# Kernel tuning notes

Hardware: AMD Instinct MI355X
Metric: run time of the kernel (lower is better)

The kernel has to match this reference:

```python
import jax, jax.numpy as jnp
import numpy as np

B, H, W = 16, 256, 256
C = 64          # width
M1, M2 = 12, 12 # retained Fourier modes
FC_HID = 128


def setup_inputs() -> dict:
    key = jax.random.key(0)
    ks = jax.random.split(key, 10)
    scale = 1.0 / (C * C)
    inp = {
        "x": jax.random.normal(ks[0], (B, H, W, 1), dtype=jnp.float32),
        "fc0_w": jax.random.normal(ks[1], (1, C), dtype=jnp.float32) * (1.0 / np.sqrt(1)),
        "fc0_b": jnp.zeros((C,), dtype=jnp.float32),
        # 4 layers x {weights1, weights2} x [Cin, Cout, M1, M2] x {re, im}
        "sc_w": jax.random.uniform(ks[2], (4, 2, C, C, M1, M2, 2), dtype=jnp.float32) * scale,
        # 1x1 conv weights [layer, Cout, Cin] and biases [layer, Cout]
        "pw_w": jax.random.normal(ks[3], (4, C, C), dtype=jnp.float32) * (1.0 / np.sqrt(C)),
        "pw_b": jnp.zeros((4, C), dtype=jnp.float32),
        "fc1_w": jax.random.normal(ks[4], (C, FC_HID), dtype=jnp.float32) * (1.0 / np.sqrt(C)),
        "fc1_b": jnp.zeros((FC_HID,), dtype=jnp.float32),
        "fc2_w": jax.random.normal(ks[5], (FC_HID, 1), dtype=jnp.float32) * (1.0 / np.sqrt(FC_HID)),
        "fc2_b": jnp.zeros((1,), dtype=jnp.float32),
    }
    return inp


def _spectral_conv(x, w1, w2):
    # x: [B, C, H, W] real; w1, w2: [Cin, Cout, M1, M2] complex
    xf = jnp.fft.rfft2(x, axes=(-2, -1))                # [B, C, H, W//2+1]
    top = jnp.einsum('bixy,ioxy->boxy', xf[:, :, :M1, :M2], w1)
    bot = jnp.einsum('bixy,ioxy->boxy', xf[:, :, -M1:, :M2], w2)
    out_ft = jnp.zeros((x.shape[0], w1.shape[1], x.shape[2], x.shape[3] // 2 + 1),
                       dtype=jnp.complex64)
    out_ft = out_ft.at[:, :, :M1, :M2].set(top)
    out_ft = out_ft.at[:, :, -M1:, :M2].set(bot)
    return jnp.fft.irfft2(out_ft, s=(x.shape[2], x.shape[3]), axes=(-2, -1))


def _gelu(x):
    return jax.nn.gelu(x, approximate=False)  # torch F.gelu default = exact erf


def reference(x, fc0_w, fc0_b, sc_w, pw_w, pw_b, fc1_w, fc1_b, fc2_w, fc2_b):
    # lift: [B,H,W,1] -> [B,H,W,C] -> [B,C,H,W]
    h = jnp.einsum('bhwi,ic->bhwc', x, fc0_w) + fc0_b
    h = jnp.transpose(h, (0, 3, 1, 2))
    scw = sc_w[..., 0] + 1j * sc_w[..., 1]  # [4, 2, C, C, M1, M2] complex
    for l in range(4):
        x1 = _spectral_conv(h, scw[l, 0], scw[l, 1])
        x2 = jnp.einsum('bihw,oi->bohw', h, pw_w[l]) + pw_b[l][None, :, None, None]
        h = x1 + x2
        if l < 3:
            h = _gelu(h)
    h = jnp.transpose(h, (0, 2, 3, 1))  # [B,H,W,C]
    h = _gelu(jnp.einsum('bhwc,cd->bhwd', h, fc1_w) + fc1_b)
    out = jnp.einsum('bhwd,do->bhwo', h, fc2_w) + fc2_b
    return out
```

## Files before the change

kernel.cpp:

```cpp
#include <hip/hip_runtime.h>
#include <hip/hip_bf16.h>
#include <math.h>

#define Hn 256
#define Wn 256
#define Cn 64
#define Mk 12
#define NM 24
#define FCH 128
#define HW 65536

using half8 = __attribute__((ext_vector_type(8))) _Float16;
using f32x4 = __attribute__((ext_vector_type(4))) float;

__device__ __forceinline__ float gelu_exact(float x) {
    return 0.5f * x * (1.0f + erff(x * 0.7071067811865476f));
}
__device__ __forceinline__ unsigned short f2h(float f) {
    _Float16 h = (_Float16)f;
    return __builtin_bit_cast(unsigned short, h);
}

__global__ __launch_bounds__(256) void k_init_tables(float* tc, float* ts,
                                                     float* twc, float* tws,
                                                     float* tcs,
                                                     unsigned short* bfr,
                                                     unsigned short* tfr) {
    int i = threadIdx.x;
    const float step = 0.024543692606170259f;
    float c = cosf(i * step), s = sinf(i * step);
    tc[i] = c; ts[i] = s;
    tcs[2 * i] = c; tcs[2 * i + 1] = s;
    for (int k = 0; k < Mk; ++k) {
        int idx = (i * k) & 255;
        twc[i * Mk + k] = cosf(idx * step);
        tws[i * Mk + k] = sinf(idx * step);
    }
    for (int e = i; e < 8192; e += 256) {
        int j  = e & 7;
        int l  = (e >> 3) & 63;
        int sn = e >> 9;
        int col = (sn & 1) * 16 + (l & 15);
        int ky = col >> 1, p = col & 1;
        int k  = (sn >> 1) * 32 + ((l >> 4) & 3) * 8 + j;
        int idx = (ky * k) & 255;
        float v = p ? -sinf(idx * step) : cosf(idx * step);
        bfr[e] = f2h(v);
    }
    for (int e = i; e < 12288; e += 256) {
        int j  = e & 7;
        int l  = (e >> 3) & 63;
        int sm = e >> 9;
        int mt = sm % 3, s2 = sm / 3;
        int r  = mt * 16 + (l & 15);
        int hh = s2 * 32 + ((l >> 4) & 3) * 8 + j;
        int m  = (r < 24) ? r : (r - 24);
        int kx = (m < Mk) ? m : (232 + m);
        int idx = (kx * hh) & 255;
        float v = (r < 24) ? cosf(idx * step) : sinf(idx * step);
        tfr[e] = f2h(v);
    }
}

__global__ __launch_bounds__(256) void k_prep_frag(const float* __restrict__ pww,
                                                   const float* __restrict__ fc1w,
                                                   unsigned short* __restrict__ efr,
                                                   unsigned short* __restrict__ pwfr,
                                                   unsigned short* __restrict__ fc1fr) {
    int e = blockIdx.x * 256 + threadIdx.x;
    const float step = 0.024543692606170259f;
    int j = e & 7, l = (e >> 3) & 63;
    int row = l & 15;
    int k = ((l >> 4) & 3) * 8 + j;
    if (e < 8192) {
        int mt = (e >> 9) & 15;
        int pix = mt * 16 + row;
        float v = 0.f;
        if (k < 12) v = cosf(((k * pix) & 255) * step);
        else if (k < 24) v = -sinf((((k - 12) * pix) & 255) * step);
        efr[e] = f2h(v);
    } else if (e < 24576) {
        int e2 = e - 8192;
        int nt = (e2 >> 9) & 3;
        int ks = (e2 >> 11) & 1;
        int l4 = e2 >> 12;
        int o = nt * 16 + row;
        int i = ks * 32 + k;
        pwfr[e2] = f2h(pww[(size_t)(l4 * 64 + o) * 64 + i]);
    } else {
        int e2 = e - 24576;
        int nt = (e2 >> 9) & 7;
        int ks = (e2 >> 12) & 1;
        int d = nt * 16 + row;
        int i = ks * 32 + k;
        fc1fr[e2] = f2h(fc1w[i * 128 + d]);
    }
}

__global__ __launch_bounds__(256) void k_prep_wfrag(const float* __restrict__ scw,
                                                    unsigned short* __restrict__ wfr) {
    __shared__ float Ws[8192];
    int mat = blockIdx.x;
    int lj = mat / 144, kxw = (mat / 12) % 12, ky = mat % 12;
    int t = threadIdx.x;
    const float* base = scw + (((size_t)lj * 4096) * 144 + kxw * 12 + ky) * 2;
#pragma unroll
    for (int r = 0; r < 16; ++r) {
        int idx = r * 256 + t;
        float2 v = *(const float2*)(base + (size_t)idx * 288);
        Ws[idx * 2] = v.x; Ws[idx * 2 + 1] = v.y;
    }
    __syncthreads();
    unsigned short* dst = wfr + (size_t)mat * 16384;
#pragma unroll
    for (int u = 0; u < 8; ++u) {
        int lin = u * 256 + t;
        int lane = lin & 63, nt = (lin >> 6) & 7, s = lin >> 9;
        int col = nt * 16 + (lane & 15);
        int o = col >> 1, pp = col & 1;
        int tg = (lane >> 4) & 3;
        unsigned pk[4];
#pragma unroll
        for (int jp = 0; jp < 4; ++jp) {
            unsigned short hv[2];
#pragma unroll
            for (int hz = 0; hz < 2; ++hz) {
                int k = s * 32 + tg * 8 + jp * 2 + hz;
                int i = k >> 1, p = k & 1;
                float wr_ = Ws[(i * 64 + o) * 2];
                float wi_ = Ws[(i * 64 + o) * 2 + 1];
                float v = (p == 0) ? (pp == 0 ? wr_ : wi_)
                                   : (pp == 0 ? -wi_ : wr_);
                hv[hz] = f2h(v);
            }
            pk[jp] = hv[0] | ((unsigned)hv[1] << 16);
        }
        uint4 w4 = {pk[0], pk[1], pk[2], pk[3]};
        *(uint4*)(dst + lin * 8) = w4;
    }
}

__global__ __launch_bounds__(64) void k_dftw_x(const float* __restrict__ x,
                                               float* __restrict__ Xxw,
                                               const float* __restrict__ twc,
                                               const float* __restrict__ tws) {
    int r = blockIdx.x * 64 + threadIdx.x;
    const float* hp = x + (size_t)r * Wn;
    float xr[Mk], xi[Mk];
#pragma unroll
    for (int k = 0; k < Mk; ++k) { xr[k] = 0.f; xi[k] = 0.f; }
    for (int w4 = 0; w4 < 64; ++w4) {
        float4 v = ((const float4*)hp)[w4];
        float vv[4] = {v.x, v.y, v.z, v.w};
#pragma unroll
        for (int j = 0; j < 4; ++j) {
            int wbase = (w4 * 4 + j) * Mk;
#pragma unroll
            for (int k = 0; k < Mk; ++k) {
                xr[k] += vv[j] * twc[wbase + k];
                xi[k] -= vv[j] * tws[wbase + k];
            }
        }
    }
    float* op = Xxw + (size_t)r * (2 * Mk);
#pragma unroll
    for (int k = 0; k < Mk; ++k) { op[2 * k] = xr[k]; op[2 * k + 1] = xi[k]; }
}

__global__ __launch_bounds__(256) void k_xdfth(const float* __restrict__ Xxw,
                                               float* __restrict__ Xfx,
                                               const float* __restrict__ tc,
                                               const float* __restrict__ ts) {
    int t = blockIdx.x * 256 + threadIdx.x;
    if (t >= 16 * 288) return;
    int ky = t % Mk;
    int m  = (t / Mk) % NM;
    int b  = t / 288;
    int kx = (m < Mk) ? m : (232 + m);
    const float* base = Xxw + (size_t)b * Hn * 2 * Mk + 2 * ky;
    float ar = 0.f, ai = 0.f;
    for (int hh = 0; hh < Hn; ++hh) {
        float vr = base[hh * 2 * Mk];
        float vi = base[hh * 2 * Mk + 1];
        int idx = (kx * hh) & 255;
        float c = tc[idx], s = ts[idx];
        ar += vr * c + vi * s;
        ai += vi * c - vr * s;
    }
    Xfx[2 * t] = ar;
    Xfx[2 * t + 1] = ai;
}

__global__ __launch_bounds__(256) void k_mixZ2(const float* __restrict__ xin,
                                               const unsigned short* __restrict__ wfr,
                                               const float* __restrict__ w0,
                                               const float* __restrict__ b0v,
                                               float* __restrict__ Z,
                                               int l, int first, int b0, int bc) {
    __shared__ __align__(16) char smem[4096];
    int t = threadIdx.x;
    int lane = t & 63, q = t >> 6, tg = (lane >> 4) & 3;
    int blk2 = blockIdx.x;
    int hlf = blk2 & 1;
    int blk = blk2 >> 1;
    int jj = blk / 144, kxw = (blk / 12) % 12, ky = blk % 12;
    int mm = jj * 12 + kxw;
    int mk = mm * 12 + ky;
    int mat = (l * 2 + jj) * 144 + kxw * 12 + ky;
    {
        int b = t >> 4, c16 = t & 15;
        uint4 pk = {0u, 0u, 0u, 0u};
        if (b < bc) {
            if (first) {
                float xr = xin[((b0 + b) * 288 + mk) * 2] * 0.0625f;
                float xi = xin[((b0 + b) * 288 + mk) * 2 + 1] * 0.0625f;
                float4 wv = *(const float4*)(w0 + c16 * 4);
                float4 bv = {0.f, 0.f, 0.f, 0.f};
                if (mk == 0) {
                    float4 bb = *(const float4*)(b0v + c16 * 4);
                    bv.x = 4096.f * bb.x; bv.y = 4096.f * bb.y;
                    bv.z = 4096.f * bb.z; bv.w = 4096.f * bb.w;
                }
                pk.x = f2h(wv.x * xr + bv.x) | ((unsigned)f2h(wv.x * xi) << 16);
                pk.y = f2h(wv.y * xr + bv.y) | ((unsigned)f2h(wv.y * xi) << 16);
                pk.z = f2h(wv.z * xr + bv.z) | ((unsigned)f2h(wv.z * xi) << 16);
                pk.w = f2h(wv.w * xr + bv.w) | ((unsigned)f2h(wv.w * xi) << 16);
            } else {
                const float* src = xin + ((size_t)b * 288 + mk) * 128 + c16 * 8;
                float4 v0 = *(const float4*)(src);
                float4 v1 = *(const float4*)(src + 4);
                pk.x = f2h(v0.x * 0.0625f) | ((unsigned)f2h(v0.y * 0.0625f) << 16);
                pk.y = f2h(v0.z * 0.0625f) | ((unsigned)f2h(v0.w * 0.0625f) << 16);
                pk.z = f2h(v1.x * 0.0625f) | ((unsigned)f2h(v1.y * 0.0625f) << 16);
                pk.w = f2h(v1.z * 0.0625f) | ((unsigned)f2h(v1.w * 0.0625f) << 16);
            }
        }
        *(uint4*)(smem + ((b * 256 + c16 * 16) ^ ((b & 7) << 4))) = pk;
    }
    __syncthreads();
    int nt = hlf * 4 + q;
    const uint4* bt = (const uint4*)wfr + (size_t)mat * 2048;
    f32x4 ac = {0.f, 0.f, 0.f, 0.f};
    int brow = lane & 15;
#pragma unroll
    for (int s = 0; s < 4; ++s) {
        half8 af = *(const half8*)(smem + ((brow * 256 + s * 64 + tg * 16) ^ ((brow & 7) << 4)));
        half8 bf = __builtin_bit_cast(half8, bt[(s * 8 + nt) * 64 + lane]);
        ac = __builtin_amdgcn_mfma_f32_16x16x32_f16(af, bf, ac, 0, 0, 0);
    }
    const float sc = 16.0f * 2.0f / 65536.0f;
    int col = nt * 16 + (lane & 15);
    int o = col >> 1, pp = col & 1;
#pragma unroll
    for (int r = 0; r < 4; ++r) {
        int bb = (lane >> 4) * 4 + r;
        if (bb < bc)
            Z[(((size_t)bb * 12 + ky) * 64 + o) * 48 + mm * 2 + pp] = ac[r] * sc;
    }
}

__global__ __launch_bounds__(256) void k_dfth(const float* __restrict__ Xw,
                                              float* __restrict__ Xf2,
                                              const unsigned short* __restrict__ tfr) {
    __shared__ __align__(16) char smem[65536];
    int b = blockIdx.x / 12, ky = blockIdx.x % 12;
    int t = threadIdx.x;
    int lane = t & 63, q = t >> 6;
    const float* P = Xw + ((size_t)b * 12 + ky) * 32768;
    int c = lane;
#pragma unroll 4
    for (int k = 0; k < 32; ++k) {
        int hh0 = k * 8 + q * 2;
        float2 a  = *(const float2*)(P + hh0 * 128 + 2 * c);
        float2 bv = *(const float2*)(P + (hh0 + 1) * 128 + 2 * c);
        unsigned int u0 = f2h(a.x * 0.0625f) | ((unsigned int)f2h(bv.x * 0.0625f) << 16);
        unsigned int u1 = f2h(a.y * 0.0625f) | ((unsigned int)f2h(bv.y * 0.0625f) << 16);
        int ch0 = 2 * c, ch1 = 2 * c + 1;
        *(unsigned int*)(smem + ch0 * 512 + ((2 * hh0) ^ ((ch0 & 7) << 4))) = u0;
        *(unsigned int*)(smem + ch1 * 512 + ((2 * hh0) ^ ((ch1 & 7) << 4))) = u1;
    }
    __syncthreads();
    int ct0 = q * 2;
    int tg = (lane >> 4) & 3;
    f32x4 a00 = {0,0,0,0}, a01 = {0,0,0,0}, a10 = {0,0,0,0};
    f32x4 a11 = {0,0,0,0}, a20 = {0,0,0,0}, a21 = {0,0,0,0};
    const uint4* tf4 = (const uint4*)tfr;
#pragma unroll
    for (int s = 0; s < 8; ++s) {
        half8 af0 = __builtin_bit_cast(half8, tf4[(s * 3 + 0) * 64 + lane]);
        half8 af1 = __builtin_bit_cast(half8, tf4[(s * 3 + 1) * 64 + lane]);
        half8 af2 = __builtin_bit_cast(half8, tf4[(s * 3 + 2) * 64 + lane]);
        int chan0 = ct0 * 16 + (lane & 15);
        int chan1 = chan0 + 16;
        int off = s * 64 + tg * 16;
        half8 b0 = *(const half8*)(smem + chan0 * 512 + (off ^ ((chan0 & 7) << 4)));
        half8 b1 = *(const half8*)(smem + chan1 * 512 + (off ^ ((chan1 & 7) << 4)));
        a00 = __builtin_amdgcn_mfma_f32_16x16x32_f16(af0, b0, a00, 0, 0, 0);
        a01 = __builtin_amdgcn_mfma_f32_16x16x32_f16(af0, b1, a01, 0, 0, 0);
        a10 = __builtin_amdgcn_mfma_f32_16x16x32_f16(af1, b0, a10, 0, 0, 0);
        a11 = __builtin_amdgcn_mfma_f32_16x16x32_f16(af1, b1, a11, 0, 0, 0);
        a20 = __builtin_amdgcn_mfma_f32_16x16x32_f16(af2, b0, a20, 0, 0, 0);
        a21 = __builtin_amdgcn_mfma_f32_16x16x32_f16(af2, b1, a21, 0, 0, 0);
    }
    __syncthreads();
    float* Cs = (float*)smem;
    {
        int rl = (lane >> 4) * 4;
        int chan0 = ct0 * 16 + (lane & 15);
#pragma unroll
        for (int r = 0; r < 4; ++r) {
            Cs[(0  + rl + r) * 128 + chan0]      = a00[r];
            Cs[(0  + rl + r) * 128 + chan0 + 16] = a01[r];
            Cs[(16 + rl + r) * 128 + chan0]      = a10[r];
            Cs[(16 + rl + r) * 128 + chan0 + 16] = a11[r];
            Cs[(32 + rl + r) * 128 + chan0]      = a20[r];
            Cs[(32 + rl + r) * 128 + chan0 + 16] = a21[r];
        }
    }
    __syncthreads();
#pragma unroll
    for (int k = 0; k < 6; ++k) {
        int p = t + 256 * k;
        int m = p >> 6, i = p & 63;
        float r1 = Cs[m * 128 + 2 * i];
        float i1 = Cs[m * 128 + 2 * i + 1];
        float r2 = Cs[(24 + m) * 128 + 2 * i];
        float i2 = Cs[(24 + m) * 128 + 2 * i + 1];
        ((float2*)Xf2)[((size_t)b * 288 + m * 12 + ky) * 64 + i] =
            make_float2((r1 + i2) * 16.0f, (i1 - r2) * 16.0f);
    }
}

__global__ __launch_bounds__(256, 4) void k_fusedA(const float* __restrict__ x0,
        const unsigned short* hin,
        const float* __restrict__ Zb, const float* __restrict__ pwb,
        const float* __restrict__ w0, const float* __restrict__ b0v,
        unsigned short* hout, float* __restrict__ XwOut,
        const float* __restrict__ tcs,
        const unsigned short* __restrict__ bfr,
        const unsigned short* __restrict__ efr,
        const unsigned short* __restrict__ pwfr,
        int l, int first) {
    __shared__ __align__(16) char smem[37120];
    float* Ysh = (float*)smem;
    char*  Yfr = smem + 32768;
    float* csm = (float*)(smem + 36864);
    int b  = blockIdx.x >> 8;
    int hh = blockIdx.x & 255;
    int w  = threadIdx.x;
    int lane = w & 63, q = w >> 6;
    int tg = (lane >> 4) & 3;
    const float2* tc2 = (const float2*)tcs;
    if (w < NM) {
        int kx = (w < Mk) ? w : (232 + w);
        float2 cs = tc2[(kx * hh) & 255];
        csm[2 * w] = cs.x; csm[2 * w + 1] = cs.y;
    }
    __syncthreads();
    const float* Zbb = Zb + (size_t)b * 36864;
    const float4* cs4 = (const float4*)csm;
#pragma unroll
    for (int r3 = 0; r3 < 3; ++r3) {
        int p = w + 256 * r3;
        int o = p / Mk, ky = p % Mk;
        const float4* zv = (const float4*)(Zbb + ((size_t)ky * 64 + o) * 48);
        float yr = 0.f, yi = 0.f;
#pragma unroll
        for (int mm = 0; mm < 12; ++mm) {
            float4 z  = zv[mm];
            float4 cc = cs4[mm];
            yr += z.x * cc.x - z.y * cc.y + z.z * cc.z - z.w * cc.w;
            yi += z.x * cc.y + z.y * cc.x + z.z * cc.w + z.w * cc.z;
        }
        Ysh[p * 2] = yr; Ysh[p * 2 + 1] = yi;
    }
    __syncthreads();
    {
        int o = q * 16 + (lane & 15);
        unsigned pv[4];
#pragma unroll
        for (int jp = 0; jp < 4; ++jp) {
            unsigned short h2[2];
#pragma unroll
            for (int hzz = 0; hzz < 2; ++hzz) {
                int u = tg * 8 + jp * 2 + hzz;
                float v;
                if (u == 0) v = 0.5f * Ysh[o * 24];
                else if (u < 12) v = Ysh[o * 24 + 2 * u];
                else if (u < 24) v = Ysh[o * 24 + 2 * (u - 12) + 1];
                else v = 0.f;
                h2[hzz] = f2h(v);
            }
            pv[jp] = h2[0] | ((unsigned)h2[1] << 16);
        }
        uint4 pk = {pv[0], pv[1], pv[2], pv[3]};
        *(uint4*)(Yfr + (q * 64 + lane) * 16) = pk;
    }
    __syncthreads();
    {
        int swz = (w & 7) << 4;
        if (first) {
            float xv = x0[(size_t)b * HW + hh * 256 + w];
#pragma unroll
            for (int ic = 0; ic < 4; ++ic) {
                unsigned pv[8];
#pragma unroll
                for (int j2 = 0; j2 < 16; j2 += 2) {
                    float a0 = w0[ic * 16 + j2] * xv + b0v[ic * 16 + j2];
                    float a1 = w0[ic * 16 + j2 + 1] * xv + b0v[ic * 16 + j2 + 1];
                    pv[j2 >> 1] = f2h(a0) | ((unsigned)f2h(a1) << 16);
                }
                uint4 lo = {pv[0], pv[1], pv[2], pv[3]};
                uint4 hi = {pv[4], pv[5], pv[6], pv[7]};
                *(uint4*)(smem + ((w * 128 + ic * 32) ^ swz)) = lo;
                *(uint4*)(smem + ((w * 128 + ic * 32 + 16) ^ swz)) = hi;
            }
        } else {
            const unsigned short* hb = hin + (size_t)b * Cn * HW + hh * 256 + w;
#pragma unroll
            for (int ic = 0; ic < 4; ++ic) {
                unsigned pv[8];
#pragma unroll
                for (int j2 = 0; j2 < 16; j2 += 2) {
                    unsigned a0 = hb[(size_t)(ic * 16 + j2) * HW];
                    unsigned a1 = hb[(size_t)(ic * 16 + j2 + 1) * HW];
                    pv[j2 >> 1] = a0 | (a1 << 16);
                }
                uint4 lo = {pv[0], pv[1], pv[2], pv[3]};
                uint4 hi = {pv[4], pv[5], pv[6], pv[7]};
                *(uint4*)(smem + ((w * 128 + ic * 32) ^ swz)) = lo;
                *(uint4*)(smem + ((w * 128 + ic * 32 + 16) ^ swz)) = hi;
            }
        }
    }
    __syncthreads();
    uint2 gp[4][4];
    {
        const uint4* efr4 = (const uint4*)efr;
        const uint4* pw4  = (const uint4*)pwfr;
        float biasn[4];
        half8 ybf[4]; uint4 cwa[4], cwb[4];
#pragma unroll
        for (int nt = 0; nt < 4; ++nt) {
            biasn[nt] = pwb[l * 64 + nt * 16 + (lane & 15)];
            ybf[nt] = *(const half8*)(Yfr + (nt * 64 + lane) * 16);
            cwa[nt] = pw4[((l * 2 + 0) * 4 + nt) * 64 + lane];
            cwb[nt] = pw4[((l * 2 + 1) * 4 + nt) * 64 + lane];
        }
#pragma unroll
        for (int mt = 0; mt < 4; ++mt) {
            int mtA = q * 4 + mt;
            half8 ea = __builtin_bit_cast(half8, efr4[mtA * 64 + lane]);
            int row = mtA * 16 + (lane & 15);
            int rsw = (row & 7) << 4;
            half8 a0 = *(const half8*)(smem + ((row * 128 + tg * 16) ^ rsw));
            half8 a1 = *(const half8*)(smem + ((row * 128 + 64 + tg * 16) ^ rsw));
#pragma unroll
            for (int nt = 0; nt < 4; ++nt) {
                f32x4 acc = {0.f, 0.f, 0.f, 0.f};
                acc = __builtin_amdgcn_mfma_f32_16x16x32_f16(ea, ybf[nt], acc, 0, 0, 0);
                acc = __builtin_amdgcn_mfma_f32_16x16x32_f16(a0, __builtin_bit_cast(half8, cwa[nt]), acc, 0, 0, 0);
                acc = __builtin_amdgcn_mfma_f32_16x16x32_f16(a1, __builtin_bit_cast(half8, cwb[nt]), acc, 0, 0, 0);
                float g0 = gelu_exact(acc[0] + biasn[nt]);
                float g1 = gelu_exact(acc[1] + biasn[nt]);
                float g2 = gelu_exact(acc[2] + biasn[nt]);
                float g3 = gelu_exact(acc[3] + biasn[nt]);
                gp[mt][nt].x = f2h(g0) | ((unsigned)f2h(g1) << 16);
                gp[mt][nt].y = f2h(g2) | ((unsigned)f2h(g3) << 16);
            }
        }
    }
    unsigned short* hnb = hout + (size_t)b * Cn * HW + hh * 256;
#pragma unroll
    for (int mt = 0; mt < 4; ++mt) {
        int pbase = (q * 4 + mt) * 16 + (lane >> 4) * 4;
#pragma unroll
        for (int nt = 0; nt < 4; ++nt) {
            int o = nt * 16 + (lane & 15);
            *(uint2*)(hnb + (size_t)o * HW + pbase) = gp[mt][nt];
        }
    }
    __syncthreads();
#pragma unroll
    for (int mt = 0; mt < 4; ++mt) {
        int pbase = (q * 4 + mt) * 16 + (lane >> 4) * 4;
#pragma unroll
        for (int nt = 0; nt < 4; ++nt) {
            int o = nt * 16 + (lane & 15);
            int sidx = (((pbase >> 3) ^ (o & 7)) << 3) | (pbase & 7);
            *(uint2*)(smem + o * 512 + sidx * 2) = gp[mt][nt];
        }
    }
    __syncthreads();
    {
        int arow = q * 16 + (lane & 15);
        const uint4* bt = (const uint4*)bfr;
        f32x4 ac0 = {0.f, 0.f, 0.f, 0.f};
        f32x4 ac1 = {0.f, 0.f, 0.f, 0.f};
#pragma unroll
        for (int s = 0; s < 8; ++s) {
            int abyte = (arow * 512 + s * 64 + tg * 16) ^ ((arow & 7) << 4);
            half8 af = __builtin_bit_cast(half8, *(const uint4*)(smem + abyte));
            half8 b0 = __builtin_bit_cast(half8, bt[(s * 2 + 0) * 64 + lane]);
            half8 b1 = __builtin_bit_cast(half8, bt[(s * 2 + 1) * 64 + lane]);
            ac0 = __builtin_amdgcn_mfma_f32_16x16x32_f16(af, b0, ac0, 0, 0, 0);
            ac1 = __builtin_amdgcn_mfma_f32_16x16x32_f16(af, b1, ac1, 0, 0, 0);
        }
        float* Xwb = XwOut + (size_t)b * 393216;
        int rbase = q * 16 + (lane >> 4) * 4;
#pragma unroll
        for (int n = 0; n < 2; ++n) {
            f32x4 ac = n ? ac1 : ac0;
            int col = n * 16 + (lane & 15);
            int ky = col >> 1, p = col & 1;
            if (ky < Mk) {
                float* dst = Xwb + (size_t)ky * 32768 + hh * 128 + rbase * 2 + p;
                dst[0] = ac[0]; dst[2] = ac[1]; dst[4] = ac[2]; dst[6] = ac[3];
            }
        }
    }
}

__global__ __launch_bounds__(256, 4) void k_fusedB(const unsigned short* __restrict__ hin,
        const float* __restrict__ Zb, const float* __restrict__ pwb,
        const float* __restrict__ fc1b, const float* __restrict__ fc2w,
        const float* __restrict__ fc2b, float* __restrict__ outp,
        const float* __restrict__ tcs,
        const unsigned short* __restrict__ efr,
        const unsigned short* __restrict__ pwfr,
        const unsigned short* __restrict__ fc1fr) {
    __shared__ __align__(16) char smem[37120];
    float* Ysh = (float*)smem;
    char*  Yfr = smem + 32768;
    float* csm = (float*)(smem + 36864);
    int b  = blockIdx.x >> 8;
    int hh = blockIdx.x & 255;
    int w  = threadIdx.x;
    int lane = w & 63, q = w >> 6;
    int tg = (lane >> 4) & 3;
    const float2* tc2 = (const float2*)tcs;
    if (w < NM) {
        int kx = (w < Mk) ? w : (232 + w);
        float2 cs = tc2[(kx * hh) & 255];
        csm[2 * w] = cs.x; csm[2 * w + 1] = cs.y;
    }
    __syncthreads();
    const float* Zbb = Zb + (size_t)b * 36864;
    const float4* cs4 = (const float4*)csm;
#pragma unroll
    for (int r3 = 0; r3 < 3; ++r3) {
        int p = w + 256 * r3;
        int o = p / Mk, ky = p % Mk;
        const float4* zv = (const float4*)(Zbb + ((size_t)ky * 64 + o) * 48);
        float yr = 0.f, yi = 0.f;
#pragma unroll
        for (int mm = 0; mm < 12; ++mm) {
            float4 z  = zv[mm];
            float4 cc = cs4[mm];
            yr += z.x * cc.x - z.y * cc.y + z.z * cc.z - z.w * cc.w;
            yi += z.x * cc.y + z.y * cc.x + z.z * cc.w + z.w * cc.z;
        }
        Ysh[p * 2] = yr; Ysh[p * 2 + 1] = yi;
    }
    __syncthreads();
    {
        int o = q * 16 + (lane & 15);
        unsigned pv[4];
#pragma unroll
        for (int jp = 0; jp < 4; ++jp) {
            unsigned short h2[2];
#pragma unroll
            for (int hzz = 0; hzz < 2; ++hzz) {
                int u = tg * 8 + jp * 2 + hzz;
                float v;
                if (u == 0) v = 0.5f * Ysh[o * 24];
                else if (u < 12) v = Ysh[o * 24 + 2 * u];
                else if (u < 24) v = Ysh[o * 24 + 2 * (u - 12) + 1];
                else v = 0.f;
                h2[hzz] = f2h(v);
            }
            pv[jp] = h2[0] | ((unsigned)h2[1] << 16);
        }
        uint4 pk = {pv[0], pv[1], pv[2], pv[3]};
        *(uint4*)(Yfr + (q * 64 + lane) * 16) = pk;
    }
    __syncthreads();
    {
        int swz = (w & 7) << 4;
        const unsigned short* hb = hin + (size_t)b * Cn * HW + hh * 256 + w;
#pragma unroll
        for (int ic = 0; ic < 4; ++ic) {
            unsigned pv[8];
#pragma unroll
            for (int j2 = 0; j2 < 16; j2 += 2) {
                unsigned a0 = hb[(size_t)(ic * 16 + j2) * HW];
                unsigned a1 = hb[(size_t)(ic * 16 + j2 + 1) * HW];
                pv[j2 >> 1] = a0 | (a1 << 16);
            }
            uint4 lo = {pv[0], pv[1], pv[2], pv[3]};
            uint4 hi = {pv[4], pv[5], pv[6], pv[7]};
            *(uint4*)(smem + ((w * 128 + ic * 32) ^ swz)) = lo;
            *(uint4*)(smem + ((w * 128 + ic * 32 + 16) ^ swz)) = hi;
        }
    }
    __syncthreads();
    uint2 R2[16];
    {
        const uint4* efr4 = (const uint4*)efr;
        const uint4* pw4 = (const uint4*)pwfr;
        half8 ay  = *(const half8*)(Yfr + (q * 64 + lane) * 16);
        half8 aw0 = __builtin_bit_cast(half8, pw4[((3 * 2 + 0) * 4 + q) * 64 + lane]);
        half8 aw1 = __builtin_bit_cast(half8, pw4[((3 * 2 + 1) * 4 + q) * 64 + lane]);
        int obase = q * 16 + (lane >> 4) * 4;
        float4 bias4 = *(const float4*)(pwb + 3 * 64 + obase);
#pragma unroll
        for (int nt = 0; nt < 16; ++nt) {
            half8 eb = __builtin_bit_cast(half8, efr4[nt * 64 + lane]);
            int pix = nt * 16 + (lane & 15);
            int psw = (pix & 7) << 4;
            half8 b0 = *(const half8*)(smem + ((pix * 128 + tg * 16) ^ psw));
            half8 b1 = *(const half8*)(smem + ((pix * 128 + 64 + tg * 16) ^ psw));
            f32x4 acc = {0.f, 0.f, 0.f, 0.f};
            acc = __builtin_amdgcn_mfma_f32_16x16x32_f16(ay, eb, acc, 0, 0, 0);
            acc = __builtin_amdgcn_mfma_f32_16x16x32_f16(aw0, b0, acc, 0, 0, 0);
            acc = __builtin_amdgcn_mfma_f32_16x16x32_f16(aw1, b1, acc, 0, 0, 0);
            R2[nt].x = f2h(acc[0] + bias4.x) | ((unsigned)f2h(acc[1] + bias4.y) << 16);
            R2[nt].y = f2h(acc[2] + bias4.z) | ((unsigned)f2h(acc[3] + bias4.w) << 16);
        }
    }
    __syncthreads();
    {
        int obase = q * 16 + (lane >> 4) * 4;
#pragma unroll
        for (int nt = 0; nt < 16; ++nt) {
            int pix = nt * 16 + (lane & 15);
            *(uint2*)(smem + ((pix * 128 + obase * 2) ^ ((pix & 7) << 4))) = R2[nt];
        }
    }
    __syncthreads();
    const uint4* f14 = (const uint4*)fc1fr;
    float w2v[8], fb1[8];
#pragma unroll
    for (int nt = 0; nt < 8; ++nt) {
        w2v[nt] = fc2w[nt * 16 + (lane & 15)];
        fb1[nt] = fc1b[nt * 16 + (lane & 15)];
    }
    float fb = fc2b[0];
    float* ob = outp + (size_t)b * HW + hh * 256;
#pragma unroll
    for (int mt = 0; mt < 4; ++mt) {
        int mtA = q * 4 + mt;
        int row = mtA * 16 + (lane & 15);
        int rsw = (row & 7) << 4;
        half8 a0 = *(const half8*)(smem + ((row * 128 + tg * 16) ^ rsw));
        half8 a1 = *(const half8*)(smem + ((row * 128 + 64 + tg * 16) ^ rsw));
        float s0 = 0.f, s1 = 0.f, s2 = 0.f, s3 = 0.f;
#pragma unroll
        for (int nt = 0; nt < 8; ++nt) {
            f32x4 acc = {0.f, 0.f, 0.f, 0.f};
            acc = __builtin_amdgcn_mfma_f32_16x16x32_f16(a0, __builtin_bit_cast(half8, f14[(0 * 8 + nt) * 64 + lane]), acc, 0, 0, 0);
            acc = __builtin_amdgcn_mfma_f32_16x16x32_f16(a1, __builtin_bit_cast(half8, f14[(1 * 8 + nt) * 64 + lane]), acc, 0, 0, 0);
            s0 += gelu_exact(acc[0] + fb1[nt]) * w2v[nt];
            s1 += gelu_exact(acc[1] + fb1[nt]) * w2v[nt];
            s2 += gelu_exact(acc[2] + fb1[nt]) * w2v[nt];
            s3 += gelu_exact(acc[3] + fb1[nt]) * w2v[nt];
        }
#pragma unroll
        for (int msk = 1; msk <= 8; msk <<= 1) {
            s0 += __shfl_xor(s0, msk);
            s1 += __shfl_xor(s1, msk);
            s2 += __shfl_xor(s2, msk);
            s3 += __shfl_xor(s3, msk);
        }
        int cc = lane & 15;
        if (cc < 4) {
            float v = (cc == 0) ? s0 : (cc == 1) ? s1 : (cc == 2) ? s2 : s3;
            ob[mtA * 16 + (lane >> 4) * 4 + cc] = v + fb;
        }
    }
}

extern "C" void kernel_launch(void* const* d_in, const int* in_sizes, int n_in,
                              void* d_out, int out_size, void* d_ws, size_t ws_size,
                              hipStream_t stream) {
    const float* x    = (const float*)d_in[0];
    const float* fc0w = (const float*)d_in[1];
    const float* fc0b = (const float*)d_in[2];
    const float* scw  = (const float*)d_in[3];
    const float* pww  = (const float*)d_in[4];
    const float* pwb  = (const float*)d_in[5];
    const float* fc1w = (const float*)d_in[6];
    const float* fc1b = (const float*)d_in[7];
    const float* fc2w = (const float*)d_in[8];
    const float* fc2b = (const float*)d_in[9];
    float* out = (float*)d_out;
    float* ws  = (float*)d_ws;

    const size_t basef = 9578496;
    const size_t perbf = 2564096;
    int bc = 0;
    for (int cand = 16; cand >= 1; cand >>= 1)
        if ((basef + perbf * (size_t)cand) * 4 <= ws_size) { bc = cand; break; }
    if (bc == 0) return;

    float* tabc = ws;
    float* tabs = tabc + 256;
    float* twc  = tabs + 256;
    float* tws_ = twc + 3072;
    float* tcs  = tws_ + 3072;
    float* bfr  = tcs + 512;
    float* tfr  = bfr + 4096;
    float* efr  = tfr + 6144;
    float* pwfr = efr + 4096;
    float* fc1f = pwfr + 8192;
    float* Xfx  = fc1f + 4096;
    float* wfr  = Xfx + 9216;
    float* Xxw  = wfr + 9437184;
    float* hbuf = ws + basef;
    unsigned short* h16 = (unsigned short*)hbuf;
    float* Xw   = hbuf + (size_t)bc * 2097152;
    float* Zb   = Xw + (size_t)bc * 393216;
    float* Xf2  = Zb + (size_t)bc * 36864;

    k_init_tables<<<1, 256, 0, stream>>>(tabc, tabs, twc, tws_, tcs,
                                         (unsigned short*)bfr,
                                         (unsigned short*)tfr);
    k_prep_frag<<<128, 256, 0, stream>>>(pww, fc1w,
                                         (unsigned short*)efr,
                                         (unsigned short*)pwfr,
                                         (unsigned short*)fc1f);
    k_prep_wfrag<<<1152, 256, 0, stream>>>(scw, (unsigned short*)wfr);
    k_dftw_x<<<64, 64, 0, stream>>>(x, Xxw, twc, tws_);
    k_xdfth<<<18, 256, 0, stream>>>(Xxw, Xfx, tabc, tabs);

    for (int b0 = 0; b0 < 16; b0 += bc) {
        k_mixZ2<<<576, 256, 0, stream>>>(Xfx, (const unsigned short*)wfr,
                                         fc0w, fc0b, Zb, 0, 1, b0, bc);
        k_fusedA<<<bc * 256, 256, 0, stream>>>(x + (size_t)b0 * HW, h16, Zb, pwb,
                                               fc0w, fc0b, h16, Xw, tcs,
                                               (const unsigned short*)bfr,
                                               (const unsigned short*)efr,
                                               (const unsigned short*)pwfr, 0, 1);
        for (int l = 1; l <= 2; ++l) {
            k_dfth<<<bc * 12, 256, 0, stream>>>(Xw, Xf2, (const unsigned short*)tfr);
            k_mixZ2<<<576, 256, 0, stream>>>(Xf2, (const unsigned short*)wfr,
                                             fc0w, fc0b, Zb, l, 0, b0, bc);
            k_fusedA<<<bc * 256, 256, 0, stream>>>(x, h16, Zb, pwb,
                                                   fc0w, fc0b, h16, Xw, tcs,
                                                   (const unsigned short*)bfr,
                                                   (const unsigned short*)efr,
                                                   (const unsigned short*)pwfr, l, 0);
        }
        k_dfth<<<bc * 12, 256, 0, stream>>>(Xw, Xf2, (const unsigned short*)tfr);
        k_mixZ2<<<576, 256, 0, stream>>>(Xf2, (const unsigned short*)wfr,
                                         fc0w, fc0b, Zb, 3, 0, b0, bc);
        k_fusedB<<<bc * 256, 256, 0, stream>>>(h16, Zb, pwb, fc1b, fc2w, fc2b,
                                               out + (size_t)b0 * HW, tcs,
                                               (const unsigned short*)efr,
                                               (const unsigned short*)pwfr,
                                               (const unsigned short*)fc1f);
    }
}
```

Measured before the change: 1.577 ms.

## Precompute inverse-H DFT per row via MFMA kernel and store Xw in fp16

Moves the per-row inverse DFT along H, which turns spectral coefficients Z into per-row Y fragments, out of k_fusedA/k_fusedB and into a new k_prepY kernel. That kernel does the work as an MFMA matmul against a precomputed cos/sin table and writes fp16 Y fragments that the fused kernels load directly. This removes the redundant scalar recomputation that each of the 256 row-blocks did, along with three syncthreads and some shared memory. It also stores the W-DFT intermediate Xw in fp16 in a planar re/im layout, halving its traffic into k_dfth. The cost is an extra kernel launch per layer, a 1 MB-per-batch Y buffer round-trip through global memory, and some added fp16 rounding.

```diff
diff --git a/kernel.cpp b/kernel.cpp
--- a/kernel.cpp
+++ b/kernel.cpp
@@ -25,7 +25,8 @@
                                                      float* twc, float* tws,
                                                      float* tcs,
                                                      unsigned short* bfr,
-                                                     unsigned short* tfr) {
+                                                     unsigned short* tfr,
+                                                     unsigned short* yfrA) {
     int i = threadIdx.x;
     const float step = 0.024543692606170259f;
     float c = cosf(i * step), s = sinf(i * step);
@@ -59,6 +60,22 @@
         int idx = (kx * hh) & 255;
         float v = (r < 24) ? cosf(idx * step) : sinf(idx * step);
         tfr[e] = f2h(v);
+    }
+    for (int e = i; e < 16384; e += 256) {
+        int j  = e & 7;
+        int l  = (e >> 3) & 63;
+        int sm = e >> 9;
+        int mt = sm & 15, s2 = sm >> 4;
+        int hh = mt * 16 + (l & 15);
+        int k  = s2 * 32 + ((l >> 4) & 3) * 8 + j;
+        int m = k >> 1, sgn = k & 1;
+        float v = 0.f;
+        if (m < 24) {
+            int kx = (m < Mk) ? m : (232 + m);
+            int idx = (kx * hh) & 255;
+            v = sgn ? sinf(idx * step) : cosf(idx * step);
+        }
+        yfrA[e] = f2h(v);
     }
 }
 
@@ -259,22 +276,91 @@
     }
 }
 
-__global__ __launch_bounds__(256) void k_dfth(const float* __restrict__ Xw,
+__global__ __launch_bounds__(256) void k_prepY(const float* __restrict__ Z,
+                                               const unsigned short* __restrict__ yfrA,
+                                               unsigned short* __restrict__ Ybuf) {
+    __shared__ __align__(16) unsigned short bf[8192];
+    int blkb = blockIdx.x / 12, ky = blockIdx.x % 12;
+    int t = threadIdx.x;
+    int lane = t & 63, q = t >> 6;
+    const float* Zbb = Z + ((size_t)blkb * 12 + ky) * 3072;
+#pragma unroll
+    for (int u4 = 0; u4 < 4; ++u4) {
+        int lin = u4 * 256 + t;
+        int lane_ = lin & 63, nt_ = (lin >> 6) & 7, s_ = lin >> 9;
+        int tg_ = (lane_ >> 4) & 3;
+        int col = nt_ * 16 + (lane_ & 15);
+        int o = col >> 1, sy = col & 1;
+        int kbase = s_ * 32 + tg_ * 8;
+        uint4 pk = {0u, 0u, 0u, 0u};
+        if (kbase < 48) {
+            const float* zp = Zbb + o * 48 + kbase;
+            float4 z0 = *(const float4*)zp;
+            float4 z1 = *(const float4*)(zp + 4);
+            float zv[8] = {z0.x, z0.y, z0.z, z0.w, z1.x, z1.y, z1.z, z1.w};
+            unsigned pv[4];
+#pragma unroll
+            for (int jp = 0; jp < 4; ++jp) {
+                float v0, v1;
+                if (sy == 0) { v0 = zv[2 * jp];     v1 = -zv[2 * jp + 1]; }
+                else         { v0 = zv[2 * jp + 1]; v1 = zv[2 * jp]; }
+                pv[jp] = f2h(v0) | ((unsigned)f2h(v1) << 16);
+            }
+            pk.x = pv[0]; pk.y = pv[1]; pk.z = pv[2]; pk.w = pv[3];
+        }
+        *(uint4*)(bf + lin * 8) = pk;
+    }
+    __syncthreads();
+    const uint4* A4 = (const uint4*)yfrA;
+    const uint4* B4 = (const uint4*)bf;
+    unsigned short* Yb = Ybuf + (size_t)blkb * 524288;
+    float dcs = (ky == 0) ? 0.5f : 1.0f;
+#pragma unroll
+    for (int mtl = 0; mtl < 4; ++mtl) {
+        int mt = q * 4 + mtl;
+        half8 a0 = __builtin_bit_cast(half8, A4[(0 * 16 + mt) * 64 + lane]);
+        half8 a1 = __builtin_bit_cast(half8, A4[(1 * 16 + mt) * 64 + lane]);
+#pragma unroll
+        for (int nt_ = 0; nt_ < 8; ++nt_) {
+            f32x4 acc = {0.f, 0.f, 0.f, 0.f};
+            acc = __builtin_amdgcn_mfma_f32_16x16x32_f16(a0,
+                    __builtin_bit_cast(half8, B4[(0 * 8 + nt_) * 64 + lane]), acc, 0, 0, 0);
+            acc = __builtin_amdgcn_mfma_f32_16x16x32_f16(a1,
+                    __builtin_bit_cast(half8, B4[(1 * 8 + nt_) * 64 + lane]), acc, 0, 0, 0);
+            int col = nt_ * 16 + (lane & 15);
+            int o = col >> 1, sy = col & 1;
+            int u = ky + 12 * sy;
+            float sc2 = (sy == 0) ? dcs : 1.0f;
+            int rbase = mt * 16 + (lane >> 4) * 4;
+#pragma unroll
+            for (int r = 0; r < 4; ++r)
+                Yb[((size_t)(rbase + r) * 64 + o) * 32 + u] = f2h(acc[r] * sc2);
+        }
+    }
+    if (ky == 0) {
+        uint4 z4 = {0u, 0u, 0u, 0u};
+        for (int e = t; e < 16384; e += 256)
+            *(uint4*)(Yb + (size_t)e * 32 + 24) = z4;
+    }
+}
+
+__global__ __launch_bounds__(256) void k_dfth(const unsigned short* __restrict__ Xw,
                                               float* __restrict__ Xf2,
                                               const unsigned short* __restrict__ tfr) {
     __shared__ __align__(16) char smem[65536];
     int b = blockIdx.x / 12, ky = blockIdx.x % 12;
     int t = threadIdx.x;
     int lane = t & 63, q = t >> 6;
-    const float* P = Xw + ((size_t)b * 12 + ky) * 32768;
+    const unsigned short* Pre = Xw + ((size_t)b * 24 + ky * 2) * 16384;
+    const unsigned short* Pim = Pre + 16384;
     int c = lane;
 #pragma unroll 4
     for (int k = 0; k < 32; ++k) {
         int hh0 = k * 8 + q * 2;
-        float2 a  = *(const float2*)(P + hh0 * 128 + 2 * c);
-        float2 bv = *(const float2*)(P + (hh0 + 1) * 128 + 2 * c);
-        unsigned int u0 = f2h(a.x * 0.0625f) | ((unsigned int)f2h(bv.x * 0.0625f) << 16);
-        unsigned int u1 = f2h(a.y * 0.0625f) | ((unsigned int)f2h(bv.y * 0.0625f) << 16);
+        unsigned r0 = Pre[hh0 * 64 + c], r1 = Pre[(hh0 + 1) * 64 + c];
+        unsigned i0 = Pim[hh0 * 64 + c], i1 = Pim[(hh0 + 1) * 64 + c];
+        unsigned u0 = r0 | (r1 << 16);
+        unsigned u1 = i0 | (i1 << 16);
         int ch0 = 2 * c, ch1 = 2 * c + 1;
         *(unsigned int*)(smem + ch0 * 512 + ((2 * hh0) ^ ((ch0 & 7) << 4))) = u0;
         *(unsigned int*)(smem + ch1 * 512 + ((2 * hh0) ^ ((ch1 & 7) << 4))) = u1;
@@ -332,71 +418,20 @@
 }
 
 __global__ __launch_bounds__(256, 4) void k_fusedA(const float* __restrict__ x0,
-        const unsigned short* hin,
-        const float* __restrict__ Zb, const float* __restrict__ pwb,
+        const unsigned short* hin, const unsigned short* __restrict__ Ybuf,
+        const float* __restrict__ pwb,
         const float* __restrict__ w0, const float* __restrict__ b0v,
-        unsigned short* hout, float* __restrict__ XwOut,
-        const float* __restrict__ tcs,
+        unsigned short* hout, unsigned short* __restrict__ XwOut,
         const unsigned short* __restrict__ bfr,
         const unsigned short* __restrict__ efr,
         const unsigned short* __restrict__ pwfr,
         int l, int first) {
-    __shared__ __align__(16) char smem[37120];
-    float* Ysh = (float*)smem;
-    char*  Yfr = smem + 32768;
-    float* csm = (float*)(smem + 36864);
+    __shared__ __align__(16) char smem[32768];
     int b  = blockIdx.x >> 8;
     int hh = blockIdx.x & 255;
     int w  = threadIdx.x;
     int lane = w & 63, q = w >> 6;
     int tg = (lane >> 4) & 3;
-    const float2* tc2 = (const float2*)tcs;
-    if (w < NM) {
-        int kx = (w < Mk) ? w : (232 + w);
-        float2 cs = tc2[(kx * hh) & 255];
-        csm[2 * w] = cs.x; csm[2 * w + 1] = cs.y;
-    }
-    __syncthreads();
-    const float* Zbb = Zb + (size_t)b * 36864;
-    const float4* cs4 = (const float4*)csm;
-#pragma unroll
-    for (int r3 = 0; r3 < 3; ++r3) {
-        int p = w + 256 * r3;
-        int o = p / Mk, ky = p % Mk;
-        const float4* zv = (const float4*)(Zbb + ((size_t)ky * 64 + o) * 48);
-        float yr = 0.f, yi = 0.f;
-#pragma unroll
-        for (int mm = 0; mm < 12; ++mm) {
-            float4 z  = zv[mm];
-            float4 cc = cs4[mm];
-            yr += z.x * cc.x - z.y * cc.y + z.z * cc.z - z.w * cc.w;
-            yi += z.x * cc.y + z.y * cc.x + z.z * cc.w + z.w * cc.z;
-        }
-        Ysh[p * 2] = yr; Ysh[p * 2 + 1] = yi;
-    }
-    __syncthreads();
-    {
-        int o = q * 16 + (lane & 15);
-        unsigned pv[4];
-#pragma unroll
-        for (int jp = 0; jp < 4; ++jp) {
-            unsigned short h2[2];
-#pragma unroll
-            for (int hzz = 0; hzz < 2; ++hzz) {
-                int u = tg * 8 + jp * 2 + hzz;
-                float v;
-                if (u == 0) v = 0.5f * Ysh[o * 24];
-                else if (u < 12) v = Ysh[o * 24 + 2 * u];
-                else if (u < 24) v = Ysh[o * 24 + 2 * (u - 12) + 1];
-                else v = 0.f;
-                h2[hzz] = f2h(v);
-            }
-            pv[jp] = h2[0] | ((unsigned)h2[1] << 16);
-        }
-        uint4 pk = {pv[0], pv[1], pv[2], pv[3]};
-        *(uint4*)(Yfr + (q * 64 + lane) * 16) = pk;
-    }
-    __syncthreads();
     {
         int swz = (w & 7) << 4;
         if (first) {
@@ -438,12 +473,14 @@
     {
         const uint4* efr4 = (const uint4*)efr;
         const uint4* pw4  = (const uint4*)pwfr;
+        const uint4* Y4 = (const uint4*)Ybuf + ((size_t)b * 256 + hh) * 256;
         float biasn[4];
         half8 ybf[4]; uint4 cwa[4], cwb[4];
 #pragma unroll
         for (int nt = 0; nt < 4; ++nt) {
-            biasn[nt] = pwb[l * 64 + nt * 16 + (lane & 15)];
-            ybf[nt] = *(const half8*)(Yfr + (nt * 64 + lane) * 16);
+            int o = nt * 16 + (lane & 15);
+            biasn[nt] = pwb[l * 64 + o];
+            ybf[nt] = __builtin_bit_cast(half8, Y4[o * 4 + tg]);
             cwa[nt] = pw4[((l * 2 + 0) * 4 + nt) * 64 + lane];
             cwb[nt] = pw4[((l * 2 + 1) * 4 + nt) * 64 + lane];
         }
@@ -506,7 +543,7 @@
             ac0 = __builtin_amdgcn_mfma_f32_16x16x32_f16(af, b0, ac0, 0, 0, 0);
             ac1 = __builtin_amdgcn_mfma_f32_16x16x32_f16(af, b1, ac1, 0, 0, 0);
         }
-        float* Xwb = XwOut + (size_t)b * 393216;
+        unsigned short* Xwb = XwOut + (size_t)b * 393216;
         int rbase = q * 16 + (lane >> 4) * 4;
 #pragma unroll
         for (int n = 0; n < 2; ++n) {
@@ -514,77 +551,28 @@
             int col = n * 16 + (lane & 15);
             int ky = col >> 1, p = col & 1;
             if (ky < Mk) {
-                float* dst = Xwb + (size_t)ky * 32768 + hh * 128 + rbase * 2 + p;
-                dst[0] = ac[0]; dst[2] = ac[1]; dst[4] = ac[2]; dst[6] = ac[3];
+                uint2 pk;
+                pk.x = f2h(ac[0] * 0.0625f) | ((unsigned)f2h(ac[1] * 0.0625f) << 16);
+                pk.y = f2h(ac[2] * 0.0625f) | ((unsigned)f2h(ac[3] * 0.0625f) << 16);
+                *(uint2*)(Xwb + ((size_t)(ky * 2 + p) * 256 + hh) * 64 + rbase) = pk;
             }
         }
     }
 }
 
 __global__ __launch_bounds__(256, 4) void k_fusedB(const unsigned short* __restrict__ hin,
-        const float* __restrict__ Zb, const float* __restrict__ pwb,
+        const unsigned short* __restrict__ Ybuf, const float* __restrict__ pwb,
         const float* __restrict__ fc1b, const float* __restrict__ fc2w,
         const float* __restrict__ fc2b, float* __restrict__ outp,
-        const float* __restrict__ tcs,
         const unsigned short* __restrict__ efr,
         const unsigned short* __restrict__ pwfr,
         const unsigned short* __restrict__ fc1fr) {
-    __shared__ __align__(16) char smem[37120];
-    float* Ysh = (float*)smem;
-    char*  Yfr = smem + 32768;
-    float* csm = (float*)(smem + 36864);
+    __shared__ __align__(16) char smem[32768];
     int b  = blockIdx.x >> 8;
     int hh = blockIdx.x & 255;
     int w  = threadIdx.x;
     int lane = w & 63, q = w >> 6;
     int tg = (lane >> 4) & 3;
-    const float2* tc2 = (const float2*)tcs;
-    if (w < NM) {
-        int kx = (w < Mk) ? w : (232 + w);
-        float2 cs = tc2[(kx * hh) & 255];
-        csm[2 * w] = cs.x; csm[2 * w + 1] = cs.y;
-    }
-    __syncthreads();
-    const float* Zbb = Zb + (size_t)b * 36864;
-    const float4* cs4 = (const float4*)csm;
-#pragma unroll
-    for (int r3 = 0; r3 < 3; ++r3) {
-        int p = w + 256 * r3;
-        int o = p / Mk, ky = p % Mk;
-        const float4* zv = (const float4*)(Zbb + ((size_t)ky * 64 + o) * 48);
-        float yr = 0.f, yi = 0.f;
-#pragma unroll
-        for (int mm = 0; mm < 12; ++mm) {
-            float4 z  = zv[mm];
-            float4 cc = cs4[mm];
-            yr += z.x * cc.x - z.y * cc.y + z.z * cc.z - z.w * cc.w;
-            yi += z.x * cc.y + z.y * cc.x + z.z * cc.w + z.w * cc.z;
-        }
-        Ysh[p * 2] = yr; Ysh[p * 2 + 1] = yi;
-    }
-    __syncthreads();
-    {
-        int o = q * 16 + (lane & 15);
-        unsigned pv[4];
-#pragma unroll
-        for (int jp = 0; jp < 4; ++jp) {
-            unsigned short h2[2];
-#pragma unroll
-            for (int hzz = 0; hzz < 2; ++hzz) {
-                int u = tg * 8 + jp * 2 + hzz;
-                float v;
-                if (u == 0) v = 0.5f * Ysh[o * 24];
-                else if (u < 12) v = Ysh[o * 24 + 2 * u];
-                else if (u < 24) v = Ysh[o * 24 + 2 * (u - 12) + 1];
-                else v = 0.f;
-                h2[hzz] = f2h(v);
-            }
-            pv[jp] = h2[0] | ((unsigned)h2[1] << 16);
-        }
-        uint4 pk = {pv[0], pv[1], pv[2], pv[3]};
-        *(uint4*)(Yfr + (q * 64 + lane) * 16) = pk;
-    }
-    __syncthreads();
     {
         int swz = (w & 7) << 4;
         const unsigned short* hb = hin + (size_t)b * Cn * HW + hh * 256 + w;
@@ -608,7 +596,8 @@
     {
         const uint4* efr4 = (const uint4*)efr;
         const uint4* pw4 = (const uint4*)pwfr;
-        half8 ay  = *(const half8*)(Yfr + (q * 64 + lane) * 16);
+        const uint4* Y4 = (const uint4*)Ybuf + ((size_t)b * 256 + hh) * 256;
+        half8 ay  = __builtin_bit_cast(half8, Y4[(q * 16 + (lane & 15)) * 4 + tg]);
         half8 aw0 = __builtin_bit_cast(half8, pw4[((3 * 2 + 0) * 4 + q) * 64 + lane]);
         half8 aw1 = __builtin_bit_cast(half8, pw4[((3 * 2 + 1) * 4 + q) * 64 + lane]);
         int obase = q * 16 + (lane >> 4) * 4;
@@ -696,8 +685,8 @@
     float* out = (float*)d_out;
     float* ws  = (float*)d_ws;
 
-    const size_t basef = 9578496;
-    const size_t perbf = 2564096;
+    const size_t basef = 9586688;
+    const size_t perbf = 2629632;
     int bc = 0;
     for (int cand = 16; cand >= 1; cand >>= 1)
         if ((basef + perbf * (size_t)cand) * 4 <= ws_size) { bc = cand; break; }
@@ -710,21 +699,24 @@
     float* tcs  = tws_ + 3072;
     float* bfr  = tcs + 512;
     float* tfr  = bfr + 4096;
-    float* efr  = tfr + 6144;
+    float* yfrA = tfr + 6144;
+    float* efr  = yfrA + 8192;
     float* pwfr = efr + 4096;
     float* fc1f = pwfr + 8192;
     float* Xfx  = fc1f + 4096;
     float* wfr  = Xfx + 9216;
     float* Xxw  = wfr + 9437184;
     float* hbuf = ws + basef;
-    unsigned short* h16 = (unsigned short*)hbuf;
-    float* Xw   = hbuf + (size_t)bc * 2097152;
-    float* Zb   = Xw + (size_t)bc * 393216;
+    unsigned short* h16  = (unsigned short*)hbuf;
+    unsigned short* Xw16 = (unsigned short*)(hbuf + (size_t)bc * 2097152);
+    float* Zb   = hbuf + (size_t)bc * (2097152 + 196608);
     float* Xf2  = Zb + (size_t)bc * 36864;
+    unsigned short* Ybuf = (unsigned short*)(Xf2 + (size_t)bc * 36864);
 
     k_init_tables<<<1, 256, 0, stream>>>(tabc, tabs, twc, tws_, tcs,
                                          (unsigned short*)bfr,
-                                         (unsigned short*)tfr);
+                                         (unsigned short*)tfr,
+                                         (unsigned short*)yfrA);
     k_prep_frag<<<128, 256, 0, stream>>>(pww, fc1w,
                                          (unsigned short*)efr,
                                          (unsigned short*)pwfr,
@@ -736,26 +728,29 @@
     for (int b0 = 0; b0 < 16; b0 += bc) {
         k_mixZ2<<<576, 256, 0, stream>>>(Xfx, (const unsigned short*)wfr,
                                          fc0w, fc0b, Zb, 0, 1, b0, bc);
-        k_fusedA<<<bc * 256, 256, 0, stream>>>(x + (size_t)b0 * HW, h16, Zb, pwb,
-                                               fc0w, fc0b, h16, Xw, tcs,
+        k_prepY<<<bc * 12, 256, 0, stream>>>(Zb, (const unsigned short*)yfrA, Ybuf);
+        k_fusedA<<<bc * 256, 256, 0, stream>>>(x + (size_t)b0 * HW, h16, Ybuf, pwb,
+                                               fc0w, fc0b, h16, Xw16,
                                                (const unsigned short*)bfr,
                                                (const unsigned short*)efr,
                                                (const unsigned short*)pwfr, 0, 1);
         for (int l = 1; l <= 2; ++l) {
-            k_dfth<<<bc * 12, 256, 0, stream>>>(Xw, Xf2, (const unsigned short*)tfr);
+            k_dfth<<<bc * 12, 256, 0, stream>>>(Xw16, Xf2, (const unsigned short*)tfr);
             k_mixZ2<<<576, 256, 0, stream>>>(Xf2, (const unsigned short*)wfr,
                                              fc0w, fc0b, Zb, l, 0, b0, bc);
-            k_fusedA<<<bc * 256, 256, 0, stream>>>(x, h16, Zb, pwb,
-                                                   fc0w, fc0b, h16, Xw, tcs,
+            k_prepY<<<bc * 12, 256, 0, stream>>>(Zb, (const unsigned short*)yfrA, Ybuf);
+            k_fusedA<<<bc * 256, 256, 0, stream>>>(x, h16, Ybuf, pwb,
+                                                   fc0w, fc0b, h16, Xw16,
                                                    (const unsigned short*)bfr,
                                                    (const unsigned short*)efr,
                                                    (const unsigned short*)pwfr, l, 0);
         }
-        k_dfth<<<bc * 12, 256, 0, stream>>>(Xw, Xf2, (const unsigned short*)tfr);
+        k_dfth<<<bc * 12, 256, 0, stream>>>(Xw16, Xf2, (const unsigned short*)tfr);
         k_mixZ2<<<576, 256, 0, stream>>>(Xf2, (const unsigned short*)wfr,
                                          fc0w, fc0b, Zb, 3, 0, b0, bc);
-        k_fusedB<<<bc * 256, 256, 0, stream>>>(h16, Zb, pwb, fc1b, fc2w, fc2b,
-                                               out + (size_t)b0 * HW, tcs,
+        k_prepY<<<bc * 12, 256, 0, stream>>>(Zb, (const unsigned short*)yfrA, Ybuf);
+        k_fusedB<<<bc * 256, 256, 0, stream>>>(h16, Ybuf, pwb, fc1b, fc2w, fc2b,
+                                               out + (size_t)b0 * HW,
                                                (const unsigned short*)efr,
                                                (const unsigned short*)pwfr,
                                                (const unsigned short*)fc1f);
```

Measured after the change: 1.321 ms. 1.19x faster.
